# Optimization experiments

Measured on AMD Instinct MI355X. Metric: run time of the kernel, lower is better.

## Reference

```python
import jax, jax.numpy as jnp
import numpy as np

GN_GROUPS = 8
GN_EPS = 1e-5


def setup_inputs() -> dict:
    key = jax.random.key(0)
    ks = jax.random.split(key, 6)
    B, M, C, H, W = 2, 5, 128, 256, 256
    scale = 1.0 / np.sqrt(C).astype(np.float32)
    x = jax.random.normal(ks[0], (B, M, C, H, W), jnp.float32)
    W1 = jax.random.normal(ks[1], (C, C), jnp.float32) * scale
    b1 = jax.random.normal(ks[2], (C,), jnp.float32) * 0.01
    gn_w = jnp.ones((C,), jnp.float32)
    gn_b = jnp.zeros((C,), jnp.float32)
    W2 = jax.random.normal(ks[3], (C, C), jnp.float32) * scale
    b2 = jax.random.normal(ks[4], (C,), jnp.float32) * 0.01
    temperature = jnp.full((1,), 0.07, jnp.float32)
    return {"x": x, "W1": W1, "b1": b1, "gn_w": gn_w, "gn_b": gn_b,
            "W2": W2, "b2": b2, "temperature": temperature, "window_size": 8}


def _group_norm(h, w, b):
    # h: (N, C, H, W); normalize over (C//G, H, W) per group
    N, C, H, W = h.shape
    hg = h.reshape(N, GN_GROUPS, C // GN_GROUPS, H, W)
    mu = hg.mean(axis=(2, 3, 4), keepdims=True)
    var = hg.var(axis=(2, 3, 4), keepdims=True)
    hg = (hg - mu) * jax.lax.rsqrt(var + GN_EPS)
    h = hg.reshape(N, C, H, W)
    return h * w[None, :, None, None] + b[None, :, None, None]


def reference(x, W1, b1, gn_w, gn_b, W2, b2, temperature, window_size):
    B, M, C, H, W = x.shape
    ws = window_size
    xf = x.reshape(B * M, C, H, W)
    # projector: 1x1 conv -> GroupNorm(8) -> GELU (erf) -> 1x1 conv
    h = jnp.einsum('nchw,oc->nohw', xf, W1) + b1[None, :, None, None]
    h = _group_norm(h, gn_w, gn_b)
    h = jax.nn.gelu(h, approximate=False)
    feats = jnp.einsum('nchw,oc->nohw', h, W2) + b2[None, :, None, None]
    # windowed contrastive loss
    N = B * M
    fw = feats.reshape(N, C, H // ws, ws, W // ws, ws)
    fw = fw.transpose(0, 2, 4, 3, 5, 1).reshape(N * (H // ws) * (W // ws), ws * ws, C)
    sim = jnp.einsum('bpc,bqc->bpq', fw, fw) / temperature[0]  # (Nw, P, P)
    logsm = jax.nn.log_softmax(sim, axis=-1)
    diag = jnp.diagonal(logsm, axis1=1, axis2=2)  # pos_mask selects the diagonal
    Nw = fw.shape[0]
    loss = -diag.sum() / (Nw * ws * ws)
    out = feats.reshape(B, M, C, H, W)
    return out, loss
```

## Files before the change

### kernel.cpp

```cpp
#include <hip/hip_runtime.h>
#include <hip/hip_bf16.h>
#include <math.h>

#define CH 128
#define IMGW 256
#define NIMG 10
#define HW 65536
#define FEATS_ELEMS ((size_t)NIMG*CH*HW)

typedef __attribute__((ext_vector_type(8))) short short8;
typedef __attribute__((ext_vector_type(4))) float f32x4;

#define WS_W1BF 0
#define WS_W2BF 8192
#define WS_PART 16384
#define WS_A    98304
#define WS_CC   99584
#define WS_LOSS 100864
#define WS_HT   141824

static __device__ __forceinline__ ushort f2bf(float f) {
    __hip_bfloat16 h = __float2bfloat16(f);
    return *reinterpret_cast<ushort*>(&h);
}
static __device__ __forceinline__ uint pack2(float a, float b) {
    return (uint)f2bf(a) | ((uint)f2bf(b) << 16);
}
static __device__ __forceinline__ float gelu_fast(float v) {
    float v2 = v*v;
    float z2 = v * fmaf(0.07135481627f, v2, 1.59576912161f);
    return v / (1.0f + __expf(-z2));
}
static __device__ __forceinline__ void xpose4(int lg, float& r0, float& r1,
                                              float& r2, float& r3) {
    float s0v = (lg&2) ? r0 : r2, s1v = (lg&2) ? r1 : r3;
    float u0 = __shfl_xor(s0v, 32), u1 = __shfl_xor(s1v, 32);
    if (lg&2) { r0 = u0; r1 = u1; } else { r2 = u0; r3 = u1; }
    float sA = (lg&1) ? r0 : r1; float uA = __shfl_xor(sA, 16);
    if (lg&1) r0 = uA; else r1 = uA;
    float sB = (lg&1) ? r2 : r3; float uB = __shfl_xor(sB, 16);
    if (lg&1) r2 = uB; else r3 = uB;
}

__global__ void k0_init(const float* __restrict__ W1, const float* __restrict__ W2,
                        float* __restrict__ ws) {
    int idx = blockIdx.x*256 + threadIdx.x;
    uint* w1b = (uint*)(ws + WS_W1BF);
    uint* w2b = (uint*)(ws + WS_W2BF);
    if (idx < 8192) {
        w1b[idx] = pack2(W1[2*idx], W1[2*idx+1]);
    } else {
        int j = idx - 8192;
        w2b[j] = pack2(W2[2*j], W2[2*j+1]);
    }
}

__global__ __launch_bounds__(512, 4) void k1_cache(const float* __restrict__ x,
        float* ws, const float* __restrict__ b1v) {
    __shared__ __align__(16) ushort xT[128*128];
    __shared__ float sp[32];
    const int t = threadIdx.x, b = blockIdx.x;
    const int swz = (b & 7)*640 + (b >> 3);
    const int n = swz >> 9, strip = swz & 511;
    const int h0 = (strip >> 4)*8, w0c = (strip & 15)*16;
    const int l = t & 63, wid = t >> 6;
    const int lm = l & 15, lg = l >> 4;
    const int swzl = 8*(lm&7);
    const ushort* w1b = (const ushort*)(ws + WS_W1BF);
    const int win = wid >> 2, ow = wid & 3;
    const int o0 = 32*ow, pB = win*64;

    f32x4 v[8];
    {
        const float* xb = x + (size_t)n*CH*HW + (size_t)h0*IMGW + w0c;
        const int q = lm & 3, dy = (lm >> 2) + 4*(wid >> 2);
        #pragma unroll
        for (int i = 0; i < 8; ++i) {
            int gc = (wid & 3)*8 + i;
            int c = 4*gc + lg;
            v[i] = __builtin_nontemporal_load(
                       (const f32x4*)(xb + (size_t)c*HW + dy*IMGW + 4*q));
        }
    }
    short8 af[2][4];
    #pragma unroll
    for (int ot = 0; ot < 2; ++ot)
        #pragma unroll
        for (int ks = 0; ks < 4; ++ks)
            af[ot][ks] = *(const short8*)(w1b + (size_t)(o0 + ot*16 + lm)*128 + ks*32 + 8*lg);
    float bv[2][4];
    #pragma unroll
    for (int ot = 0; ot < 2; ++ot)
        #pragma unroll
        for (int r = 0; r < 4; ++r) bv[ot][r] = b1v[o0 + ot*16 + 4*lg + r];

    {
        const int q = lm & 3, dy = (lm >> 2) + 4*(wid >> 2);
        #pragma unroll
        for (int i = 0; i < 8; ++i) {
            int gc = (wid & 3)*8 + i;
            float r0 = v[i][0], r1 = v[i][1], r2 = v[i][2], r3 = v[i][3];
            xpose4(lg, r0, r1, r2, r3);
            int col = 4*q + lg;
            int p = (col >> 3)*64 + dy*8 + (col & 7);
            uint2 pk; pk.x = pack2(r0, r1); pk.y = pack2(r2, r3);
            *(uint2*)&xT[p*128 + ((4*gc) ^ (8*(p&7)))] = pk;
        }
    }
    __syncthreads();

    f32x4 hacc[2][4];
    #pragma unroll
    for (int ot = 0; ot < 2; ++ot)
        #pragma unroll
        for (int pt = 0; pt < 4; ++pt)
            hacc[ot][pt] = (f32x4){bv[ot][0], bv[ot][1], bv[ot][2], bv[ot][3]};
    #pragma unroll
    for (int ks = 0; ks < 4; ++ks)
        #pragma unroll
        for (int pt = 0; pt < 4; ++pt) {
            short8 bfr = *(const short8*)&xT[(pB + pt*16 + lm)*128 + ((ks*32 + 8*lg) ^ swzl)];
            hacc[0][pt] = __builtin_amdgcn_mfma_f32_16x16x32_bf16(af[0][ks], bfr, hacc[0][pt], 0,0,0);
            hacc[1][pt] = __builtin_amdgcn_mfma_f32_16x16x32_bf16(af[1][ks], bfr, hacc[1][pt], 0,0,0);
        }

    float s1[2] = {0.f, 0.f}, s2[2] = {0.f, 0.f};
    #pragma unroll
    for (int ot = 0; ot < 2; ++ot)
        #pragma unroll
        for (int pt = 0; pt < 4; ++pt)
            #pragma unroll
            for (int r = 0; r < 4; ++r) {
                float h = hacc[ot][pt][r];
                s1[ot] += h; s2[ot] += h*h;
            }
    #pragma unroll
    for (int ot = 0; ot < 2; ++ot) {
        float a = s1[ot], q = s2[ot];
        #pragma unroll
        for (int off = 1; off < 64; off <<= 1) {
            a += __shfl_xor(a, off); q += __shfl_xor(q, off);
        }
        if (l == 0) { sp[wid*4 + ot*2] = a; sp[wid*4 + ot*2 + 1] = q; }
    }
    __syncthreads();

    if (t < 16) {
        int g = t & 7, which = t >> 3;
        int w0 = g >> 1, slot = (g & 1)*2 + which;
        float vv = sp[w0*4 + slot] + sp[(4 + w0)*4 + slot];
        ws[WS_PART + (size_t)swz*16 + which*8 + g] = vv;
    }

    #pragma unroll
    for (int ot = 0; ot < 2; ++ot)
        #pragma unroll
        for (int pt = 0; pt < 4; ++pt) {
            f32x4 h = hacc[ot][pt];
            int p = pB + pt*16 + lm;
            uint2 pk; pk.x = pack2(h[0], h[1]); pk.y = pack2(h[2], h[3]);
            *(uint2*)&xT[p*128 + ((o0 + ot*16 + 4*lg) ^ swzl)] = pk;
        }
    __syncthreads();

    const uint4* srcv = (const uint4*)xT;
    uint4* dstv = (uint4*)(ws + WS_HT + (size_t)swz*8192);
    #pragma unroll
    for (int i = 0; i < 4; ++i) dstv[t + i*512] = srcv[t + i*512];
}

__global__ __launch_bounds__(256) void k2_final(const float* __restrict__ gnw,
        const float* __restrict__ gnb, float* ws) {
    __shared__ float red[256];
    __shared__ float tot[16];
    __shared__ float muS[8], rsS[8];
    const int t = threadIdx.x, n = blockIdx.x;
    const int s = t & 15, i0 = t >> 4;
    const float* base = ws + WS_PART + (size_t)n*512*16;
    float p = 0.f;
    for (int k = 0; k < 32; ++k) p += base[(i0 + 16*k)*16 + s];
    red[t] = p;
    __syncthreads();
    if (t < 16) {
        float v = 0.f;
        #pragma unroll
        for (int j = 0; j < 16; ++j) v += red[j*16 + t];
        tot[t] = v;
    }
    __syncthreads();
    if (t < 8) {
        const float inv = 1.0f/1048576.0f;
        float mu  = tot[t]*inv;
        float var = tot[8 + t]*inv - mu*mu;
        muS[t] = mu; rsS[t] = rsqrtf(var + 1e-5f);
    }
    __syncthreads();
    if (t < 128) {
        int g = t >> 4;
        float a = rsS[g]*gnw[t];
        ws[WS_A  + n*128 + t] = a;
        ws[WS_CC + n*128 + t] = gnb[t] - muS[g]*a;
    }
}

__global__ __launch_bounds__(512, 4) void k3_consume(float* ws,
        const float* __restrict__ b2v, const float* __restrict__ temp,
        float* __restrict__ out) {
    __shared__ __align__(16) ushort fb[128*128];
    __shared__ __align__(16) float  st[64*136];
    const int t = threadIdx.x, b = blockIdx.x;
    const int swz = (b & 7)*640 + (b >> 3);
    const int n = swz >> 9, strip = swz & 511;
    const int h0 = (strip >> 4)*8, w0c = (strip & 15)*16;
    const int l = t & 63, wid = t >> 6;
    const int lm = l & 15, lg = l >> 4;
    const int swzl = 8*(lm&7);
    const ushort* w2b = (const ushort*)(ws + WS_W2BF);

    {
        const char* src = (const char*)(ws + WS_HT + (size_t)swz*8192);
        #pragma unroll
        for (int i = 0; i < 4; ++i) {
            __builtin_amdgcn_global_load_lds(
                (const __attribute__((address_space(1))) void*)(src + ((size_t)(t + i*512))*16),
                (__attribute__((address_space(3))) void*)&fb[(size_t)(t + i*512)*8],
                16, 0, 0);
        }
    }
    __syncthreads();

    {
        uint2* hu = (uint2*)fb;
        const float* aP = ws + WS_A  + n*128;
        const float* cP = ws + WS_CC + n*128;
        #pragma unroll
        for (int i = 0; i < 8; ++i) {
            int c0 = t + i*512;
            int p = c0 >> 5;
            int o = ((c0 & 31)*4) ^ (8*(p&7));
            uint2 v = hu[c0];
            float hv0 = __uint_as_float((v.x & 0xffffu) << 16);
            float hv1 = __uint_as_float(v.x & 0xffff0000u);
            float hv2 = __uint_as_float((v.y & 0xffffu) << 16);
            float hv3 = __uint_as_float(v.y & 0xffff0000u);
            float g0 = gelu_fast(fmaf(hv0, aP[o],   cP[o]));
            float g1 = gelu_fast(fmaf(hv1, aP[o+1], cP[o+1]));
            float g2 = gelu_fast(fmaf(hv2, aP[o+2], cP[o+2]));
            float g3 = gelu_fast(fmaf(hv3, aP[o+3], cP[o+3]));
            uint2 pk; pk.x = pack2(g0, g1); pk.y = pack2(g2, g3);
            hu[c0] = pk;
        }
    }
    __syncthreads();

    const int win = wid >> 2, ow = wid & 3;
    const int o0 = 32*ow, pB = win*64;
    const int half = ow >> 1;

    short8 af2[2][4];
    #pragma unroll
    for (int ot = 0; ot < 2; ++ot)
        #pragma unroll
        for (int ks = 0; ks < 4; ++ks)
            af2[ot][ks] = *(const short8*)(w2b + (size_t)(o0 + ot*16 + lm)*128 + ks*32 + 8*lg);
    f32x4 facc[2][4];
    #pragma unroll
    for (int ot = 0; ot < 2; ++ot)
        #pragma unroll
        for (int pt = 0; pt < 4; ++pt) facc[ot][pt] = (f32x4){0.f,0.f,0.f,0.f};
    #pragma unroll
    for (int ks = 0; ks < 4; ++ks)
        #pragma unroll
        for (int pt = 0; pt < 4; ++pt) {
            short8 bfr = *(const short8*)&fb[(pB + pt*16 + lm)*128 + ((ks*32 + 8*lg) ^ swzl)];
            facc[0][pt] = __builtin_amdgcn_mfma_f32_16x16x32_bf16(af2[0][ks], bfr, facc[0][pt], 0,0,0);
            facc[1][pt] = __builtin_amdgcn_mfma_f32_16x16x32_bf16(af2[1][ks], bfr, facc[1][pt], 0,0,0);
        }
    #pragma unroll
    for (int ot = 0; ot < 2; ++ot) {
        float b2r0 = b2v[o0 + ot*16 + 4*lg + 0], b2r1 = b2v[o0 + ot*16 + 4*lg + 1];
        float b2r2 = b2v[o0 + ot*16 + 4*lg + 2], b2r3 = b2v[o0 + ot*16 + 4*lg + 3];
        #pragma unroll
        for (int pt = 0; pt < 4; ++pt) {
            facc[ot][pt][0] += b2r0; facc[ot][pt][1] += b2r1;
            facc[ot][pt][2] += b2r2; facc[ot][pt][3] += b2r3;
        }
    }
    __syncthreads();

    #pragma unroll
    for (int ot = 0; ot < 2; ++ot)
        #pragma unroll
        for (int pt = 0; pt < 4; ++pt) {
            f32x4 f = facc[ot][pt];
            int p = pt*16 + lm;
            uint2 pk; pk.x = pack2(f[0], f[1]); pk.y = pack2(f[2], f[3]);
            *(uint2*)&fb[(pB + p)*128 + ((o0 + ot*16 + 4*lg) ^ swzl)] = pk;
        }
    if (half == 0) {
        #pragma unroll
        for (int ot = 0; ot < 2; ++ot)
            #pragma unroll
            for (int pt = 0; pt < 4; ++pt) {
                int p = pt*16 + lm, py = p >> 3, px = p & 7;
                int col = py*16 + win*8 + px;
                int cb = (ow & 1)*32 + ot*16 + 4*lg;
                f32x4 f = facc[ot][pt];
                st[(cb+0)*136 + col] = f[0];
                st[(cb+1)*136 + col] = f[1];
                st[(cb+2)*136 + col] = f[2];
                st[(cb+3)*136 + col] = f[3];
            }
    }
    __syncthreads();

    {
        #pragma unroll
        for (int i = 0; i < 4; ++i) {
            int f4 = t + i*512;
            int cl = f4 >> 5, rem = f4 & 31;
            int y = rem >> 2, xq = rem & 3;
            f32x4 val = *(const f32x4*)&st[cl*136 + y*16 + xq*4];
            __builtin_nontemporal_store(val,
                (f32x4*)(out + (size_t)n*CH*HW + (size_t)cl*HW
                             + (size_t)(h0 + y)*IMGW + w0c + xq*4));
        }
    }
    const float invT = 1.f / temp[0];
    f32x4 sacc[4];
    #pragma unroll
    for (int qt = 0; qt < 4; ++qt) sacc[qt] = (f32x4){0.f,0.f,0.f,0.f};
    #pragma unroll
    for (int ks = 0; ks < 4; ++ks) {
        short8 afr = *(const short8*)&fb[(pB + 16*ow + lm)*128 + ((ks*32 + 8*lg) ^ swzl)];
        #pragma unroll
        for (int qt = 0; qt < 4; ++qt) {
            short8 bfr = *(const short8*)&fb[(pB + qt*16 + lm)*128 + ((ks*32 + 8*lg) ^ swzl)];
            sacc[qt] = __builtin_amdgcn_mfma_f32_16x16x32_bf16(afr, bfr, sacc[qt], 0,0,0);
        }
    }
    __syncthreads();

    if (half == 1) {
        #pragma unroll
        for (int ot = 0; ot < 2; ++ot)
            #pragma unroll
            for (int pt = 0; pt < 4; ++pt) {
                int p = pt*16 + lm, py = p >> 3, px = p & 7;
                int col = py*16 + win*8 + px;
                int cb = (ow & 1)*32 + ot*16 + 4*lg;
                f32x4 f = facc[ot][pt];
                st[(cb+0)*136 + col] = f[0];
                st[(cb+1)*136 + col] = f[1];
                st[(cb+2)*136 + col] = f[2];
                st[(cb+3)*136 + col] = f[3];
            }
    }
    __syncthreads();
    {
        #pragma unroll
        for (int i = 0; i < 4; ++i) {
            int f4 = t + i*512;
            int cl = f4 >> 5, rem = f4 & 31;
            int y = rem >> 2, xq = rem & 3;
            f32x4 val = *(const f32x4*)&st[cl*136 + y*16 + xq*4];
            __builtin_nontemporal_store(val,
                (f32x4*)(out + (size_t)n*CH*HW + (size_t)(64 + cl)*HW
                             + (size_t)(h0 + y)*IMGW + w0c + xq*4));
        }
    }

    float lossAcc = 0.f;
    #pragma unroll
    for (int r = 0; r < 4; ++r) {
        float v0 = sacc[0][r]*invT, v1 = sacc[1][r]*invT;
        float v2 = sacc[2][r]*invT, v3 = sacc[3][r]*invT;
        float m = fmaxf(fmaxf(v0, v1), fmaxf(v2, v3));
        m = fmaxf(m, __shfl_xor(m, 1)); m = fmaxf(m, __shfl_xor(m, 2));
        m = fmaxf(m, __shfl_xor(m, 4)); m = fmaxf(m, __shfl_xor(m, 8));
        float s = __expf(v0-m) + __expf(v1-m) + __expf(v2-m) + __expf(v3-m);
        s += __shfl_xor(s, 1); s += __shfl_xor(s, 2);
        s += __shfl_xor(s, 4); s += __shfl_xor(s, 8);
        float lse = m + logf(s);
        if (lm == 4*lg + r) {
            float dv = (ow == 0) ? v0 : (ow == 1) ? v1 : (ow == 2) ? v2 : v3;
            lossAcc += lse - dv;
        }
    }
    lossAcc += __shfl_xor(lossAcc, 1);  lossAcc += __shfl_xor(lossAcc, 2);
    lossAcc += __shfl_xor(lossAcc, 4);  lossAcc += __shfl_xor(lossAcc, 8);
    lossAcc += __shfl_xor(lossAcc, 16); lossAcc += __shfl_xor(lossAcc, 32);
    if (l == 0) ws[WS_LOSS + (size_t)b*8 + wid] = lossAcc;
}

__global__ void k4_loss(const float* __restrict__ ws, float* __restrict__ out) {
    __shared__ float red[4];
    int t = threadIdx.x;
    float s = 0.f;
    for (int i = t; i < 40960; i += 256) s += ws[WS_LOSS + i];
    #pragma unroll
    for (int off = 32; off > 0; off >>= 1) s += __shfl_down(s, off, 64);
    if ((t & 63) == 0) red[t >> 6] = s;
    __syncthreads();
    if (t == 0) out[FEATS_ELEMS] = (red[0] + red[1] + red[2] + red[3]) * (1.f/655360.f);
}

extern "C" void kernel_launch(void* const* d_in, const int* in_sizes, int n_in,
                              void* d_out, int out_size, void* d_ws, size_t ws_size,
                              hipStream_t stream) {
    (void)in_sizes; (void)n_in; (void)out_size; (void)ws_size;
    const float* x    = (const float*)d_in[0];
    const float* W1   = (const float*)d_in[1];
    const float* b1   = (const float*)d_in[2];
    const float* gnw  = (const float*)d_in[3];
    const float* gnb  = (const float*)d_in[4];
    const float* W2   = (const float*)d_in[5];
    const float* b2   = (const float*)d_in[6];
    const float* temp = (const float*)d_in[7];
    float* out = (float*)d_out;
    float* ws  = (float*)d_ws;

    hipLaunchKernelGGL(k0_init,    dim3(64),   dim3(256), 0, stream, W1, W2, ws);
    hipLaunchKernelGGL(k1_cache,   dim3(5120), dim3(512), 0, stream, x, ws, b1);
    hipLaunchKernelGGL(k2_final,   dim3(10),   dim3(256), 0, stream, gnw, gnb, ws);
    hipLaunchKernelGGL(k3_consume, dim3(5120), dim3(512), 0, stream, ws, b2, temp, out);
    hipLaunchKernelGGL(k4_loss,    dim3(1),    dim3(256), 0, stream, ws, out);
}
```

Measured before the change: 296.8 us.

## Process two strips per block in k1 with double-buffered LDS prefetch

The first-conv kernel now handles two adjacent 16-column strips per block, which halves the grid. The second strip's global loads are issued before the MFMA work on the first strip, so memory latency overlaps with compute. Each strip gets its own LDS buffer. The cost is twice the LDS per block (about 64KB), which may lower occupancy, plus fewer blocks to fill the GPU.

After: 352.0 us. 18.6% more time.

```diff
diff --git a/kernel.cpp b/kernel.cpp
--- a/kernel.cpp
+++ b/kernel.cpp
@@ -55,32 +55,31 @@
     }
 }
 
-__global__ __launch_bounds__(512, 4) void k1_cache(const float* __restrict__ x,
+__global__ __launch_bounds__(512, 4) void k1_db(const float* __restrict__ x,
         float* ws, const float* __restrict__ b1v) {
-    __shared__ __align__(16) ushort xT[128*128];
-    __shared__ float sp[32];
+    __shared__ __align__(16) ushort xTa[128*128];
+    __shared__ __align__(16) ushort xTb[128*128];
+    __shared__ float sp[64];
     const int t = threadIdx.x, b = blockIdx.x;
-    const int swz = (b & 7)*640 + (b >> 3);
-    const int n = swz >> 9, strip = swz & 511;
-    const int h0 = (strip >> 4)*8, w0c = (strip & 15)*16;
+    const int swzp = (b & 7)*320 + (b >> 3);
+    const int sA = 2*swzp;
+    const int n = sA >> 9, stA = sA & 511;
+    const int h0 = (stA >> 4)*8, w0c = (stA & 15)*16;
     const int l = t & 63, wid = t >> 6;
     const int lm = l & 15, lg = l >> 4;
     const int swzl = 8*(lm&7);
     const ushort* w1b = (const ushort*)(ws + WS_W1BF);
     const int win = wid >> 2, ow = wid & 3;
     const int o0 = 32*ow, pB = win*64;
+    const int q = lm & 3, dy = (lm >> 2) + 4*(wid >> 2);
+    const float* xb = x + (size_t)n*CH*HW + (size_t)h0*IMGW + w0c;
 
     f32x4 v[8];
-    {
-        const float* xb = x + (size_t)n*CH*HW + (size_t)h0*IMGW + w0c;
-        const int q = lm & 3, dy = (lm >> 2) + 4*(wid >> 2);
-        #pragma unroll
-        for (int i = 0; i < 8; ++i) {
-            int gc = (wid & 3)*8 + i;
-            int c = 4*gc + lg;
-            v[i] = __builtin_nontemporal_load(
-                       (const f32x4*)(xb + (size_t)c*HW + dy*IMGW + 4*q));
-        }
+    #pragma unroll
+    for (int i = 0; i < 8; ++i) {
+        int c = 4*((wid & 3)*8 + i) + lg;
+        v[i] = __builtin_nontemporal_load(
+                   (const f32x4*)(xb + (size_t)c*HW + dy*IMGW + 4*q));
     }
     short8 af[2][4];
     #pragma unroll
@@ -94,21 +93,24 @@
         #pragma unroll
         for (int r = 0; r < 4; ++r) bv[ot][r] = b1v[o0 + ot*16 + 4*lg + r];
 
-    {
-        const int q = lm & 3, dy = (lm >> 2) + 4*(wid >> 2);
-        #pragma unroll
-        for (int i = 0; i < 8; ++i) {
-            int gc = (wid & 3)*8 + i;
-            float r0 = v[i][0], r1 = v[i][1], r2 = v[i][2], r3 = v[i][3];
-            xpose4(lg, r0, r1, r2, r3);
-            int col = 4*q + lg;
-            int p = (col >> 3)*64 + dy*8 + (col & 7);
-            uint2 pk; pk.x = pack2(r0, r1); pk.y = pack2(r2, r3);
-            *(uint2*)&xT[p*128 + ((4*gc) ^ (8*(p&7)))] = pk;
-        }
-    }
-    __syncthreads();
-
+    #pragma unroll
+    for (int i = 0; i < 8; ++i) {
+        int gc = (wid & 3)*8 + i;
+        float r0 = v[i][0], r1 = v[i][1], r2 = v[i][2], r3 = v[i][3];
+        xpose4(lg, r0, r1, r2, r3);
+        int col = 4*q + lg;
+        int p = (col >> 3)*64 + dy*8 + (col & 7);
+        uint2 pk; pk.x = pack2(r0, r1); pk.y = pack2(r2, r3);
+        *(uint2*)&xTa[p*128 + ((4*gc) ^ (8*(p&7)))] = pk;
+    }
+    __syncthreads();
+
+    #pragma unroll
+    for (int i = 0; i < 8; ++i) {
+        int c = 4*((wid & 3)*8 + i) + lg;
+        v[i] = __builtin_nontemporal_load(
+                   (const f32x4*)(xb + 16 + (size_t)c*HW + dy*IMGW + 4*q));
+    }
     f32x4 hacc[2][4];
     #pragma unroll
     for (int ot = 0; ot < 2; ++ot)
@@ -119,29 +121,40 @@
     for (int ks = 0; ks < 4; ++ks)
         #pragma unroll
         for (int pt = 0; pt < 4; ++pt) {
-            short8 bfr = *(const short8*)&xT[(pB + pt*16 + lm)*128 + ((ks*32 + 8*lg) ^ swzl)];
+            short8 bfr = *(const short8*)&xTa[(pB + pt*16 + lm)*128 + ((ks*32 + 8*lg) ^ swzl)];
             hacc[0][pt] = __builtin_amdgcn_mfma_f32_16x16x32_bf16(af[0][ks], bfr, hacc[0][pt], 0,0,0);
             hacc[1][pt] = __builtin_amdgcn_mfma_f32_16x16x32_bf16(af[1][ks], bfr, hacc[1][pt], 0,0,0);
         }
-
-    float s1[2] = {0.f, 0.f}, s2[2] = {0.f, 0.f};
-    #pragma unroll
-    for (int ot = 0; ot < 2; ++ot)
-        #pragma unroll
-        for (int pt = 0; pt < 4; ++pt)
-            #pragma unroll
-            for (int r = 0; r < 4; ++r) {
-                float h = hacc[ot][pt][r];
-                s1[ot] += h; s2[ot] += h*h;
+    {
+        float s1[2] = {0.f, 0.f}, s2[2] = {0.f, 0.f};
+        #pragma unroll
+        for (int ot = 0; ot < 2; ++ot)
+            #pragma unroll
+            for (int pt = 0; pt < 4; ++pt)
+                #pragma unroll
+                for (int r = 0; r < 4; ++r) {
+                    float h = hacc[ot][pt][r];
+                    s1[ot] += h; s2[ot] += h*h;
+                }
+        #pragma unroll
+        for (int ot = 0; ot < 2; ++ot) {
+            float a = s1[ot], qq = s2[ot];
+            #pragma unroll
+            for (int off = 1; off < 64; off <<= 1) {
+                a += __shfl_xor(a, off); qq += __shfl_xor(qq, off);
             }
-    #pragma unroll
-    for (int ot = 0; ot < 2; ++ot) {
-        float a = s1[ot], q = s2[ot];
-        #pragma unroll
-        for (int off = 1; off < 64; off <<= 1) {
-            a += __shfl_xor(a, off); q += __shfl_xor(q, off);
-        }
-        if (l == 0) { sp[wid*4 + ot*2] = a; sp[wid*4 + ot*2 + 1] = q; }
+            if (l == 0) { sp[wid*4 + ot*2] = a; sp[wid*4 + ot*2 + 1] = qq; }
+        }
+    }
+    #pragma unroll
+    for (int i = 0; i < 8; ++i) {
+        int gc = (wid & 3)*8 + i;
+        float r0 = v[i][0], r1 = v[i][1], r2 = v[i][2], r3 = v[i][3];
+        xpose4(lg, r0, r1, r2, r3);
+        int col = 4*q + lg;
+        int p = (col >> 3)*64 + dy*8 + (col & 7);
+        uint2 pk; pk.x = pack2(r0, r1); pk.y = pack2(r2, r3);
+        *(uint2*)&xTb[p*128 + ((4*gc) ^ (8*(p&7)))] = pk;
     }
     __syncthreads();
 
@@ -149,9 +162,8 @@
         int g = t & 7, which = t >> 3;
         int w0 = g >> 1, slot = (g & 1)*2 + which;
         float vv = sp[w0*4 + slot] + sp[(4 + w0)*4 + slot];
-        ws[WS_PART + (size_t)swz*16 + which*8 + g] = vv;
-    }
-
+        ws[WS_PART + (size_t)sA*16 + which*8 + g] = vv;
+    }
     #pragma unroll
     for (int ot = 0; ot < 2; ++ot)
         #pragma unroll
@@ -159,14 +171,73 @@
             f32x4 h = hacc[ot][pt];
             int p = pB + pt*16 + lm;
             uint2 pk; pk.x = pack2(h[0], h[1]); pk.y = pack2(h[2], h[3]);
-            *(uint2*)&xT[p*128 + ((o0 + ot*16 + 4*lg) ^ swzl)] = pk;
-        }
-    __syncthreads();
-
-    const uint4* srcv = (const uint4*)xT;
-    uint4* dstv = (uint4*)(ws + WS_HT + (size_t)swz*8192);
-    #pragma unroll
-    for (int i = 0; i < 4; ++i) dstv[t + i*512] = srcv[t + i*512];
+            *(uint2*)&xTa[p*128 + ((o0 + ot*16 + 4*lg) ^ swzl)] = pk;
+        }
+    #pragma unroll
+    for (int ot = 0; ot < 2; ++ot)
+        #pragma unroll
+        for (int pt = 0; pt < 4; ++pt)
+            hacc[ot][pt] = (f32x4){bv[ot][0], bv[ot][1], bv[ot][2], bv[ot][3]};
+    #pragma unroll
+    for (int ks = 0; ks < 4; ++ks)
+        #pragma unroll
+        for (int pt = 0; pt < 4; ++pt) {
+            short8 bfr = *(const short8*)&xTb[(pB + pt*16 + lm)*128 + ((ks*32 + 8*lg) ^ swzl)];
+            hacc[0][pt] = __builtin_amdgcn_mfma_f32_16x16x32_bf16(af[0][ks], bfr, hacc[0][pt], 0,0,0);
+            hacc[1][pt] = __builtin_amdgcn_mfma_f32_16x16x32_bf16(af[1][ks], bfr, hacc[1][pt], 0,0,0);
+        }
+    {
+        float s1[2] = {0.f, 0.f}, s2[2] = {0.f, 0.f};
+        #pragma unroll
+        for (int ot = 0; ot < 2; ++ot)
+            #pragma unroll
+            for (int pt = 0; pt < 4; ++pt)
+                #pragma unroll
+                for (int r = 0; r < 4; ++r) {
+                    float h = hacc[ot][pt][r];
+                    s1[ot] += h; s2[ot] += h*h;
+                }
+        #pragma unroll
+        for (int ot = 0; ot < 2; ++ot) {
+            float a = s1[ot], qq = s2[ot];
+            #pragma unroll
+            for (int off = 1; off < 64; off <<= 1) {
+                a += __shfl_xor(a, off); qq += __shfl_xor(qq, off);
+            }
+            if (l == 0) { sp[32 + wid*4 + ot*2] = a; sp[32 + wid*4 + ot*2 + 1] = qq; }
+        }
+    }
+    __syncthreads();
+
+    {
+        const uint4* srcv = (const uint4*)xTa;
+        uint4* dstv = (uint4*)(ws + WS_HT + (size_t)sA*8192);
+        #pragma unroll
+        for (int i = 0; i < 4; ++i) dstv[t + i*512] = srcv[t + i*512];
+    }
+    if (t < 16) {
+        int g = t & 7, which = t >> 3;
+        int w0 = g >> 1, slot = (g & 1)*2 + which;
+        float vv = sp[32 + w0*4 + slot] + sp[32 + (4 + w0)*4 + slot];
+        ws[WS_PART + (size_t)(sA + 1)*16 + which*8 + g] = vv;
+    }
+    #pragma unroll
+    for (int ot = 0; ot < 2; ++ot)
+        #pragma unroll
+        for (int pt = 0; pt < 4; ++pt) {
+            f32x4 h = hacc[ot][pt];
+            int p = pB + pt*16 + lm;
+            uint2 pk; pk.x = pack2(h[0], h[1]); pk.y = pack2(h[2], h[3]);
+            *(uint2*)&xTb[p*128 + ((o0 + ot*16 + 4*lg) ^ swzl)] = pk;
+        }
+    __syncthreads();
+
+    {
+        const uint4* srcv = (const uint4*)xTb;
+        uint4* dstv = (uint4*)(ws + WS_HT + (size_t)(sA + 1)*8192);
+        #pragma unroll
+        for (int i = 0; i < 4; ++i) dstv[t + i*512] = srcv[t + i*512];
+    }
 }
 
 __global__ __launch_bounds__(256) void k2_final(const float* __restrict__ gnw,
@@ -421,7 +492,7 @@
     float* ws  = (float*)d_ws;
 
     hipLaunchKernelGGL(k0_init,    dim3(64),   dim3(256), 0, stream, W1, W2, ws);
-    hipLaunchKernelGGL(k1_cache,   dim3(5120), dim3(512), 0, stream, x, ws, b1);
+    hipLaunchKernelGGL(k1_db,      dim3(2560), dim3(512), 0, stream, x, ws, b1);
     hipLaunchKernelGGL(k2_final,   dim3(10),   dim3(256), 0, stream, gnw, gnb, ws);
     hipLaunchKernelGGL(k3_consume, dim3(5120), dim3(512), 0, stream, ws, b2, temp, out);
     hipLaunchKernelGGL(k4_loss,    dim3(1),    dim3(256), 0, stream, ws, out);
```

## Split first-projection kernel into per-window 256-thread blocks for higher occupancy

Applied to the files above, without the earlier changes.

The first-stage kernel now processes one 8x8 window per 256-thread block instead of a two-window strip per 512-thread block. This halves shared memory per block and doubles the grid, so more blocks can be resident and the x loads are spread over more waves. Group-norm partial sums move to a new workspace region with twice as many entries, and the reduction kernel is updated to sum them. The output layout of the bf16 intermediate is kept, so the consumer kernel is unchanged. In exchange, each row of x is now read in 32-byte pieces instead of 64-byte pieces, and there is more per-block overhead.

After: 449.7 us. +51.5%, slower.

```diff
diff --git a/kernel.cpp b/kernel.cpp
--- a/kernel.cpp
+++ b/kernel.cpp
@@ -13,11 +13,11 @@
 
 #define WS_W1BF 0
 #define WS_W2BF 8192
-#define WS_PART 16384
 #define WS_A    98304
 #define WS_CC   99584
 #define WS_LOSS 100864
 #define WS_HT   141824
+#define WS_PART2 42084864
 
 static __device__ __forceinline__ ushort f2bf(float f) {
     __hip_bfloat16 h = __float2bfloat16(f);
@@ -55,29 +55,27 @@
     }
 }
 
-__global__ __launch_bounds__(512, 4) void k1_cache(const float* __restrict__ x,
+__global__ __launch_bounds__(256, 8) void k1_win(const float* __restrict__ x,
         float* ws, const float* __restrict__ b1v) {
-    __shared__ __align__(16) ushort xT[128*128];
-    __shared__ float sp[32];
+    __shared__ __align__(16) ushort xT[64*128];
+    __shared__ float sp[16];
     const int t = threadIdx.x, b = blockIdx.x;
-    const int swz = (b & 7)*640 + (b >> 3);
-    const int n = swz >> 9, strip = swz & 511;
-    const int h0 = (strip >> 4)*8, w0c = (strip & 15)*16;
+    const int swz = (b & 7)*1280 + (b >> 3);
+    const int n = swz >> 10, widx = swz & 1023;
+    const int h0 = (widx >> 5)*8, w0 = (widx & 31)*8;
     const int l = t & 63, wid = t >> 6;
     const int lm = l & 15, lg = l >> 4;
     const int swzl = 8*(lm&7);
     const ushort* w1b = (const ushort*)(ws + WS_W1BF);
-    const int win = wid >> 2, ow = wid & 3;
-    const int o0 = 32*ow, pB = win*64;
+    const int o0 = 32*wid;
 
     f32x4 v[8];
     {
-        const float* xb = x + (size_t)n*CH*HW + (size_t)h0*IMGW + w0c;
-        const int q = lm & 3, dy = (lm >> 2) + 4*(wid >> 2);
+        const float* xb = x + (size_t)n*CH*HW + (size_t)h0*IMGW + w0;
+        const int q = lm & 1, dy = lm >> 1;
         #pragma unroll
         for (int i = 0; i < 8; ++i) {
-            int gc = (wid & 3)*8 + i;
-            int c = 4*gc + lg;
+            int c = 4*(wid*8 + i) + lg;
             v[i] = __builtin_nontemporal_load(
                        (const f32x4*)(xb + (size_t)c*HW + dy*IMGW + 4*q));
         }
@@ -95,14 +93,13 @@
         for (int r = 0; r < 4; ++r) bv[ot][r] = b1v[o0 + ot*16 + 4*lg + r];
 
     {
-        const int q = lm & 3, dy = (lm >> 2) + 4*(wid >> 2);
+        const int q = lm & 1, dy = lm >> 1;
         #pragma unroll
         for (int i = 0; i < 8; ++i) {
-            int gc = (wid & 3)*8 + i;
+            int gc = wid*8 + i;
             float r0 = v[i][0], r1 = v[i][1], r2 = v[i][2], r3 = v[i][3];
             xpose4(lg, r0, r1, r2, r3);
-            int col = 4*q + lg;
-            int p = (col >> 3)*64 + dy*8 + (col & 7);
+            int p = dy*8 + 4*q + lg;
             uint2 pk; pk.x = pack2(r0, r1); pk.y = pack2(r2, r3);
             *(uint2*)&xT[p*128 + ((4*gc) ^ (8*(p&7)))] = pk;
         }
@@ -119,7 +116,7 @@
     for (int ks = 0; ks < 4; ++ks)
         #pragma unroll
         for (int pt = 0; pt < 4; ++pt) {
-            short8 bfr = *(const short8*)&xT[(pB + pt*16 + lm)*128 + ((ks*32 + 8*lg) ^ swzl)];
+            short8 bfr = *(const short8*)&xT[(pt*16 + lm)*128 + ((ks*32 + 8*lg) ^ swzl)];
             hacc[0][pt] = __builtin_amdgcn_mfma_f32_16x16x32_bf16(af[0][ks], bfr, hacc[0][pt], 0,0,0);
             hacc[1][pt] = __builtin_amdgcn_mfma_f32_16x16x32_bf16(af[1][ks], bfr, hacc[1][pt], 0,0,0);
         }
@@ -146,10 +143,8 @@
     __syncthreads();
 
     if (t < 16) {
-        int g = t & 7, which = t >> 3;
-        int w0 = g >> 1, slot = (g & 1)*2 + which;
-        float vv = sp[w0*4 + slot] + sp[(4 + w0)*4 + slot];
-        ws[WS_PART + (size_t)swz*16 + which*8 + g] = vv;
+        int which = t >> 3, g = t & 7;
+        ws[WS_PART2 + (size_t)swz*16 + t] = sp[(g>>1)*4 + (g&1)*2 + which];
     }
 
     #pragma unroll
@@ -157,16 +152,20 @@
         #pragma unroll
         for (int pt = 0; pt < 4; ++pt) {
             f32x4 h = hacc[ot][pt];
-            int p = pB + pt*16 + lm;
+            int p = pt*16 + lm;
             uint2 pk; pk.x = pack2(h[0], h[1]); pk.y = pack2(h[2], h[3]);
             *(uint2*)&xT[p*128 + ((o0 + ot*16 + 4*lg) ^ swzl)] = pk;
         }
     __syncthreads();
 
-    const uint4* srcv = (const uint4*)xT;
-    uint4* dstv = (uint4*)(ws + WS_HT + (size_t)swz*8192);
-    #pragma unroll
-    for (int i = 0; i < 4; ++i) dstv[t + i*512] = srcv[t + i*512];
+    {
+        const size_t strip_g = (size_t)n*512 + (size_t)(widx >> 5)*16
+                             + (size_t)((widx & 31) >> 1);
+        const uint4* srcv = (const uint4*)xT;
+        uint4* dstv = (uint4*)(ws + WS_HT + strip_g*8192 + (size_t)(widx & 1)*4096);
+        #pragma unroll
+        for (int i = 0; i < 4; ++i) dstv[t + i*256] = srcv[t + i*256];
+    }
 }
 
 __global__ __launch_bounds__(256) void k2_final(const float* __restrict__ gnw,
@@ -176,9 +175,9 @@
     __shared__ float muS[8], rsS[8];
     const int t = threadIdx.x, n = blockIdx.x;
     const int s = t & 15, i0 = t >> 4;
-    const float* base = ws + WS_PART + (size_t)n*512*16;
+    const float* base = ws + WS_PART2 + (size_t)n*1024*16;
     float p = 0.f;
-    for (int k = 0; k < 32; ++k) p += base[(i0 + 16*k)*16 + s];
+    for (int k = 0; k < 64; ++k) p += base[(i0 + 16*k)*16 + s];
     red[t] = p;
     __syncthreads();
     if (t < 16) {
@@ -420,9 +419,9 @@
     float* out = (float*)d_out;
     float* ws  = (float*)d_ws;
 
-    hipLaunchKernelGGL(k0_init,    dim3(64),   dim3(256), 0, stream, W1, W2, ws);
-    hipLaunchKernelGGL(k1_cache,   dim3(5120), dim3(512), 0, stream, x, ws, b1);
-    hipLaunchKernelGGL(k2_final,   dim3(10),   dim3(256), 0, stream, gnw, gnb, ws);
-    hipLaunchKernelGGL(k3_consume, dim3(5120), dim3(512), 0, stream, ws, b2, temp, out);
-    hipLaunchKernelGGL(k4_loss,    dim3(1),    dim3(256), 0, stream, ws, out);
-}
+    hipLaunchKernelGGL(k0_init,    dim3(64),    dim3(256), 0, stream, W1, W2, ws);
+    hipLaunchKernelGGL(k1_win,     dim3(10240), dim3(256), 0, stream, x, ws, b1);
+    hipLaunchKernelGGL(k2_final,   dim3(10),    dim3(256), 0, stream, gnw, gnb, ws);
+    hipLaunchKernelGGL(k3_consume, dim3(5120),  dim3(512), 0, stream, ws, b2, temp, out);
+    hipLaunchKernelGGL(k4_loss,    dim3(1),     dim3(256), 0, stream, ws, out);
+}
```

## Process two strips per block in first projection kernel with wider loads

Applied to the files above, without the earlier changes.

The first projection kernel now handles a 32-wide tile (two 16-wide strips) per block, halving its grid. Each thread issues 16 input loads whose lanes cover 128 contiguous bytes per row, and a transpose with different shuffle masks rearranges them. The 1x1 conv MFMA runs in two phases over shared memory that is twice as large. This doubles LDS use per block to 64KB, which may cut occupancy from the requested 4 blocks per CU. The per-group partial sums are written into the first strip's slot and the second slot is zeroed, so the later reduction stays unchanged.

New measurement: 278.0 us. -6.3%, faster.

```diff
diff --git a/kernel.cpp b/kernel.cpp
--- a/kernel.cpp
+++ b/kernel.cpp
@@ -31,15 +31,15 @@
     float z2 = v * fmaf(0.07135481627f, v2, 1.59576912161f);
     return v / (1.0f + __expf(-z2));
 }
-static __device__ __forceinline__ void xpose4(int lg, float& r0, float& r1,
-                                              float& r2, float& r3) {
-    float s0v = (lg&2) ? r0 : r2, s1v = (lg&2) ? r1 : r3;
-    float u0 = __shfl_xor(s0v, 32), u1 = __shfl_xor(s1v, 32);
-    if (lg&2) { r0 = u0; r1 = u1; } else { r2 = u0; r3 = u1; }
-    float sA = (lg&1) ? r0 : r1; float uA = __shfl_xor(sA, 16);
-    if (lg&1) r0 = uA; else r1 = uA;
-    float sB = (lg&1) ? r2 : r3; float uB = __shfl_xor(sB, 16);
-    if (lg&1) r2 = uB; else r3 = uB;
+static __device__ __forceinline__ void xpose4m(int a, int m1, int m0,
+        float& r0, float& r1, float& r2, float& r3) {
+    float s0v = (a&2) ? r0 : r2, s1v = (a&2) ? r1 : r3;
+    float u0 = __shfl_xor(s0v, m1), u1 = __shfl_xor(s1v, m1);
+    if (a&2) { r0 = u0; r1 = u1; } else { r2 = u0; r3 = u1; }
+    float sA = (a&1) ? r0 : r1; float uA = __shfl_xor(sA, m0);
+    if (a&1) r0 = uA; else r1 = uA;
+    float sB = (a&1) ? r2 : r3; float uB = __shfl_xor(sB, m0);
+    if (a&1) r2 = uB; else r3 = uB;
 }
 
 __global__ void k0_init(const float* __restrict__ W1, const float* __restrict__ W2,
@@ -55,31 +55,32 @@
     }
 }
 
-__global__ __launch_bounds__(512, 4) void k1_cache(const float* __restrict__ x,
+__global__ __launch_bounds__(512, 4) void k1_quad(const float* __restrict__ x,
         float* ws, const float* __restrict__ b1v) {
-    __shared__ __align__(16) ushort xT[128*128];
+    __shared__ __align__(16) ushort xq[256*128];
     __shared__ float sp[32];
     const int t = threadIdx.x, b = blockIdx.x;
-    const int swz = (b & 7)*640 + (b >> 3);
-    const int n = swz >> 9, strip = swz & 511;
-    const int h0 = (strip >> 4)*8, w0c = (strip & 15)*16;
+    const int qidx = (b & 7)*320 + (b >> 3);
+    const int n = qidx >> 8, rem = qidx & 255;
+    const int sr = rem >> 3, qc = rem & 7;
+    const int h0 = sr*8, w0q = qc*32;
+    const size_t g0 = (size_t)n*512 + sr*16 + 2*qc;
     const int l = t & 63, wid = t >> 6;
     const int lm = l & 15, lg = l >> 4;
     const int swzl = 8*(lm&7);
     const ushort* w1b = (const ushort*)(ws + WS_W1BF);
-    const int win = wid >> 2, ow = wid & 3;
-    const int o0 = 32*ow, pB = win*64;
-
-    f32x4 v[8];
-    {
-        const float* xb = x + (size_t)n*CH*HW + (size_t)h0*IMGW + w0c;
-        const int q = lm & 3, dy = (lm >> 2) + 4*(wid >> 2);
-        #pragma unroll
-        for (int i = 0; i < 8; ++i) {
-            int gc = (wid & 3)*8 + i;
-            int c = 4*gc + lg;
+    const int ow = wid & 3, o0 = 32*ow;
+
+    const int oct = l >> 3, j = l & 7;
+    f32x4 v[16];
+    {
+        const float* xb = x + (size_t)n*CH*HW + (size_t)h0*IMGW + w0q;
+        #pragma unroll
+        for (int i = 0; i < 16; ++i) {
+            int c = (i & 1)*64 + 8*wid + oct;
+            int dy = i >> 1;
             v[i] = __builtin_nontemporal_load(
-                       (const f32x4*)(xb + (size_t)c*HW + dy*IMGW + 4*q));
+                       (const f32x4*)(xb + (size_t)c*HW + dy*IMGW + 4*j));
         }
     }
     short8 af[2][4];
@@ -95,78 +96,87 @@
         for (int r = 0; r < 4; ++r) bv[ot][r] = b1v[o0 + ot*16 + 4*lg + r];
 
     {
-        const int q = lm & 3, dy = (lm >> 2) + 4*(wid >> 2);
-        #pragma unroll
-        for (int i = 0; i < 8; ++i) {
-            int gc = (wid & 3)*8 + i;
+        const int a = oct & 3, A = oct >> 2;
+        #pragma unroll
+        for (int i = 0; i < 16; ++i) {
             float r0 = v[i][0], r1 = v[i][1], r2 = v[i][2], r3 = v[i][3];
-            xpose4(lg, r0, r1, r2, r3);
-            int col = 4*q + lg;
-            int p = (col >> 3)*64 + dy*8 + (col & 7);
+            xpose4m(a, 16, 8, r0, r1, r2, r3);
+            int col = 4*j + a;
+            int P = (col >> 3)*64 + (i >> 1)*8 + (col & 7);
+            int cq = (i & 1)*64 + 8*wid + 4*A;
             uint2 pk; pk.x = pack2(r0, r1); pk.y = pack2(r2, r3);
-            *(uint2*)&xT[p*128 + ((4*gc) ^ (8*(p&7)))] = pk;
-        }
-    }
-    __syncthreads();
-
-    f32x4 hacc[2][4];
-    #pragma unroll
-    for (int ot = 0; ot < 2; ++ot)
-        #pragma unroll
-        for (int pt = 0; pt < 4; ++pt)
-            hacc[ot][pt] = (f32x4){bv[ot][0], bv[ot][1], bv[ot][2], bv[ot][3]};
-    #pragma unroll
-    for (int ks = 0; ks < 4; ++ks)
-        #pragma unroll
-        for (int pt = 0; pt < 4; ++pt) {
-            short8 bfr = *(const short8*)&xT[(pB + pt*16 + lm)*128 + ((ks*32 + 8*lg) ^ swzl)];
-            hacc[0][pt] = __builtin_amdgcn_mfma_f32_16x16x32_bf16(af[0][ks], bfr, hacc[0][pt], 0,0,0);
-            hacc[1][pt] = __builtin_amdgcn_mfma_f32_16x16x32_bf16(af[1][ks], bfr, hacc[1][pt], 0,0,0);
-        }
+            *(uint2*)&xq[P*128 + (cq ^ (8*(P&7)))] = pk;
+        }
+    }
+    __syncthreads();
 
     float s1[2] = {0.f, 0.f}, s2[2] = {0.f, 0.f};
     #pragma unroll
-    for (int ot = 0; ot < 2; ++ot)
-        #pragma unroll
-        for (int pt = 0; pt < 4; ++pt)
-            #pragma unroll
-            for (int r = 0; r < 4; ++r) {
-                float h = hacc[ot][pt][r];
-                s1[ot] += h; s2[ot] += h*h;
+    for (int ph = 0; ph < 2; ++ph) {
+        const int win = 2*ph + (wid >> 2);
+        f32x4 hacc[2][4];
+        #pragma unroll
+        for (int ot = 0; ot < 2; ++ot)
+            #pragma unroll
+            for (int pt = 0; pt < 4; ++pt)
+                hacc[ot][pt] = (f32x4){bv[ot][0], bv[ot][1], bv[ot][2], bv[ot][3]};
+        #pragma unroll
+        for (int ks = 0; ks < 4; ++ks)
+            #pragma unroll
+            for (int pt = 0; pt < 4; ++pt) {
+                short8 bfr = *(const short8*)&xq[(win*64 + pt*16 + lm)*128 + ((ks*32 + 8*lg) ^ swzl)];
+                hacc[0][pt] = __builtin_amdgcn_mfma_f32_16x16x32_bf16(af[0][ks], bfr, hacc[0][pt], 0,0,0);
+                hacc[1][pt] = __builtin_amdgcn_mfma_f32_16x16x32_bf16(af[1][ks], bfr, hacc[1][pt], 0,0,0);
             }
+        #pragma unroll
+        for (int ot = 0; ot < 2; ++ot)
+            #pragma unroll
+            for (int pt = 0; pt < 4; ++pt)
+                #pragma unroll
+                for (int r = 0; r < 4; ++r) {
+                    float h = hacc[ot][pt][r];
+                    s1[ot] += h; s2[ot] += h*h;
+                }
+        __syncthreads();
+        #pragma unroll
+        for (int ot = 0; ot < 2; ++ot)
+            #pragma unroll
+            for (int pt = 0; pt < 4; ++pt) {
+                f32x4 h = hacc[ot][pt];
+                int P = win*64 + pt*16 + lm;
+                uint2 pk; pk.x = pack2(h[0], h[1]); pk.y = pack2(h[2], h[3]);
+                *(uint2*)&xq[P*128 + ((o0 + ot*16 + 4*lg) ^ swzl)] = pk;
+            }
+    }
+
     #pragma unroll
     for (int ot = 0; ot < 2; ++ot) {
-        float a = s1[ot], q = s2[ot];
+        float a = s1[ot], qq = s2[ot];
         #pragma unroll
         for (int off = 1; off < 64; off <<= 1) {
-            a += __shfl_xor(a, off); q += __shfl_xor(q, off);
-        }
-        if (l == 0) { sp[wid*4 + ot*2] = a; sp[wid*4 + ot*2 + 1] = q; }
-    }
-    __syncthreads();
+            a += __shfl_xor(a, off); qq += __shfl_xor(qq, off);
+        }
+        if (l == 0) { sp[wid*4 + ot*2] = a; sp[wid*4 + ot*2 + 1] = qq; }
+    }
+    __syncthreads();
+
+    {
+        const uint4* srcv = (const uint4*)xq;
+        uint4* d0 = (uint4*)(ws + WS_HT + g0*8192);
+        uint4* d1 = (uint4*)(ws + WS_HT + (g0+1)*8192);
+        #pragma unroll
+        for (int i = 0; i < 4; ++i) d0[t + i*512] = srcv[t + i*512];
+        #pragma unroll
+        for (int i = 0; i < 4; ++i) d1[t + i*512] = srcv[2048 + t + i*512];
+    }
 
     if (t < 16) {
-        int g = t & 7, which = t >> 3;
-        int w0 = g >> 1, slot = (g & 1)*2 + which;
-        float vv = sp[w0*4 + slot] + sp[(4 + w0)*4 + slot];
-        ws[WS_PART + (size_t)swz*16 + which*8 + g] = vv;
-    }
-
-    #pragma unroll
-    for (int ot = 0; ot < 2; ++ot)
-        #pragma unroll
-        for (int pt = 0; pt < 4; ++pt) {
-            f32x4 h = hacc[ot][pt];
-            int p = pB + pt*16 + lm;
-            uint2 pk; pk.x = pack2(h[0], h[1]); pk.y = pack2(h[2], h[3]);
-            *(uint2*)&xT[p*128 + ((o0 + ot*16 + 4*lg) ^ swzl)] = pk;
-        }
-    __syncthreads();
-
-    const uint4* srcv = (const uint4*)xT;
-    uint4* dstv = (uint4*)(ws + WS_HT + (size_t)swz*8192);
-    #pragma unroll
-    for (int i = 0; i < 4; ++i) dstv[t + i*512] = srcv[t + i*512];
+        int which = t >> 3, g = t & 7;
+        int ow_ = g >> 1, ot_ = g & 1;
+        float vv = sp[ow_*4 + ot_*2 + which] + sp[(4+ow_)*4 + ot_*2 + which];
+        ws[WS_PART + g0*16 + t] = vv;
+        ws[WS_PART + (g0+1)*16 + t] = 0.0f;
+    }
 }
 
 __global__ __launch_bounds__(256) void k2_final(const float* __restrict__ gnw,
@@ -184,7 +194,7 @@
     if (t < 16) {
         float v = 0.f;
         #pragma unroll
-        for (int j = 0; j < 16; ++j) v += red[j*16 + t];
+        for (int jj = 0; jj < 16; ++jj) v += red[jj*16 + t];
         tot[t] = v;
     }
     __syncthreads();
@@ -319,11 +329,11 @@
         for (int i = 0; i < 4; ++i) {
             int f4 = t + i*512;
             int cl = f4 >> 5, rem = f4 & 31;
-            int y = rem >> 2, xq = rem & 3;
-            f32x4 val = *(const f32x4*)&st[cl*136 + y*16 + xq*4];
+            int y = rem >> 2, xq2 = rem & 3;
+            f32x4 val = *(const f32x4*)&st[cl*136 + y*16 + xq2*4];
             __builtin_nontemporal_store(val,
                 (f32x4*)(out + (size_t)n*CH*HW + (size_t)cl*HW
-                             + (size_t)(h0 + y)*IMGW + w0c + xq*4));
+                             + (size_t)(h0 + y)*IMGW + w0c + xq2*4));
         }
     }
     const float invT = 1.f / temp[0];
@@ -362,11 +372,11 @@
         for (int i = 0; i < 4; ++i) {
             int f4 = t + i*512;
             int cl = f4 >> 5, rem = f4 & 31;
-            int y = rem >> 2, xq = rem & 3;
-            f32x4 val = *(const f32x4*)&st[cl*136 + y*16 + xq*4];
+            int y = rem >> 2, xq2 = rem & 3;
+            f32x4 val = *(const f32x4*)&st[cl*136 + y*16 + xq2*4];
             __builtin_nontemporal_store(val,
                 (f32x4*)(out + (size_t)n*CH*HW + (size_t)(64 + cl)*HW
-                             + (size_t)(h0 + y)*IMGW + w0c + xq*4));
+                             + (size_t)(h0 + y)*IMGW + w0c + xq2*4));
         }
     }
 
@@ -421,7 +431,7 @@
     float* ws  = (float*)d_ws;
 
     hipLaunchKernelGGL(k0_init,    dim3(64),   dim3(256), 0, stream, W1, W2, ws);
-    hipLaunchKernelGGL(k1_cache,   dim3(5120), dim3(512), 0, stream, x, ws, b1);
+    hipLaunchKernelGGL(k1_quad,    dim3(2560), dim3(512), 0, stream, x, ws, b1);
     hipLaunchKernelGGL(k2_final,   dim3(10),   dim3(256), 0, stream, gnw, gnb, ws);
     hipLaunchKernelGGL(k3_consume, dim3(5120), dim3(512), 0, stream, ws, b2, temp, out);
     hipLaunchKernelGGL(k4_loss,    dim3(1),    dim3(256), 0, stream, ws, out);
```
